# Optimization experiments

Hardware: AMD Instinct MI355X
Metric: run time of the kernel (lower is better)

Reference implementation:

```python
import jax, jax.numpy as jnp
import numpy as np

N = 100000      # num nodes
E = 800000      # num edges
IN = 128        # in_channels
OUT = 128       # out_channels
ALPHA = 0.5


def setup_inputs() -> dict:
    key = jax.random.key(0)
    k1, k2, k3, k4, k5, k6 = jax.random.split(key, 6)
    x = jax.random.normal(k1, (N, IN), dtype=jnp.float32)
    edge_index = jax.random.randint(k2, (2, E), 0, N, dtype=jnp.int32)
    # GCNConv linear weights (glorot-ish) and biases for both directions
    s = 1.0 / np.sqrt(IN)
    W_sd = jax.random.normal(k3, (IN, OUT), dtype=jnp.float32) * s
    b_sd = jnp.zeros((OUT,), dtype=jnp.float32)
    W_ds = jax.random.normal(k4, (IN, OUT), dtype=jnp.float32) * s
    b_ds = jnp.zeros((OUT,), dtype=jnp.float32)
    return {"x": x, "edge_index": edge_index, "W_sd": W_sd, "b_sd": b_sd,
            "W_ds": W_ds, "b_ds": b_ds}


def _dir_gcn_norm_weights(row, col, dtype):
    """edge_weight = out_deg_inv_sqrt[row] * in_deg_inv_sqrt[col] (unit input weights)."""
    ones = jnp.ones((row.shape[0],), dtype=dtype)
    in_deg = jax.ops.segment_sum(ones, col, num_segments=N)
    out_deg = jax.ops.segment_sum(ones, row, num_segments=N)
    in_inv = jnp.where(in_deg > 0, jax.lax.rsqrt(in_deg), 0.0).astype(dtype)
    out_inv = jnp.where(out_deg > 0, jax.lax.rsqrt(out_deg), 0.0).astype(dtype)
    return out_inv[row] * in_inv[col]


def _gcn_conv(x, W, b, src, dst, w):
    """GCNConv(normalize=False, add_self_loops=False): lin -> gather -> scale -> scatter-add -> +bias."""
    h = x @ W                                   # [N, OUT]
    msg = h[src] * w[:, None]                   # [E, OUT]
    return jax.ops.segment_sum(msg, dst, num_segments=N) + b


def reference(x, edge_index, W_sd, b_sd, W_ds, b_ds):
    row, col = edge_index[0], edge_index[1]
    # forward-direction norm (src->dst) and transposed-graph norm (edge_index.flip(0))
    w = _dir_gcn_norm_weights(row, col, x.dtype)
    w_t = _dir_gcn_norm_weights(col, row, x.dtype)
    # conv_dst_to_src uses transposed edges: source=col, dest=row
    x_in = _gcn_conv(x, W_ds, b_ds, col, row, w_t)
    # conv_src_to_dst uses original edges: source=row, dest=col
    x_out = _gcn_conv(x, W_sd, b_sd, row, col, w)
    return ALPHA * x_in + (1.0 - ALPHA) * x_out
```

## Files before the change

### kernel.cpp

```cpp
#include <hip/hip_runtime.h>

#define NN 100000
#define NE 800000
#define NI 1600000
#define NB 391
#define IPB 6250

#define GB_CVT 12500
#define GB_PW  128
#define GB_HIST 256

#define OFF_INV    0u
#define OFF_OFFS   800000u
#define OFF_BB     1600008u
#define OFF_HIST   1601600u
#define OFF_CSRC   2001984u
#define OFF_XB     8401984u
#define OFF_PAIRS  34001984u
#define OFF_WT     85201984u
#define OFF_BIAS   85267520u
#define OFF_TOT    85268032u

typedef short short8 __attribute__((ext_vector_type(8)));
typedef unsigned short u16x8 __attribute__((ext_vector_type(8)));
typedef float f32x4 __attribute__((ext_vector_type(4)));
typedef float f32x8 __attribute__((ext_vector_type(8)));

__device__ __forceinline__ unsigned short f2bf(float f) {
    unsigned u = __float_as_uint(f);
    u = (u + 0x7FFFu + ((u >> 16) & 1u)) >> 16;
    return (unsigned short)u;
}
__device__ __forceinline__ float b2f(unsigned short h) {
    return __uint_as_float(((unsigned)h) << 16);
}
__device__ __forceinline__ f32x8 bvec2f(u16x8 v) {
    f32x8 r;
#pragma unroll
    for (int i = 0; i < 8; ++i) r[i] = b2f(v[i]);
    return r;
}


__global__ __launch_bounds__(256) void k_prep(
    const float4* __restrict__ x4, ushort4* __restrict__ xb4,
    const float* __restrict__ Wds, const float* __restrict__ Wsd,
    const float* __restrict__ bds, const float* __restrict__ bsd,
    unsigned short* __restrict__ wt, float* __restrict__ bias,
    const int* __restrict__ ei, int* __restrict__ hist) {
    __shared__ int h[NB];
    int bid = blockIdx.x;
    if (bid < GB_CVT) {
        int i = bid * 256 + threadIdx.x;
        float4 v = x4[i];
        ushort4 o;
        o.x = f2bf(v.x); o.y = f2bf(v.y); o.z = f2bf(v.z); o.w = f2bf(v.w);
        xb4[i] = o;
        return;
    }
    if (bid < GB_CVT + GB_PW) {
        int id = (bid - GB_CVT) * 256 + threadIdx.x;
        int c = id & 127;
        int k = id >> 7;
        float v = (k < 128) ? Wds[k * 128 + c] : Wsd[(k - 128) * 128 + c];
        wt[c * 256 + k] = f2bf(v);
        if (k == 0) bias[c] = 0.5f * (bds[c] + bsd[c]);
        return;
    }
    int hb = bid - GB_CVT - GB_PW;
    for (int k = threadIdx.x; k < NB; k += 256) h[k] = 0;
    __syncthreads();
    int base = hb * IPB;
    for (int t = threadIdx.x; t < IPB; t += 256) {
        int i = base + t;
        int key = (i < NE) ? ei[i] : (NN + ei[i]);
        atomicAdd(&h[key >> 9], 1);
    }
    __syncthreads();
    for (int k = threadIdx.x; k < NB; k += 256) hist[k * 256 + hb] = h[k];
}

__global__ __launch_bounds__(256) void k_red(const int* __restrict__ hist,
                                             int* __restrict__ tot) {
    __shared__ int s[256];
    int k = blockIdx.x;
    s[threadIdx.x] = hist[k * 256 + threadIdx.x];
    __syncthreads();
    for (int st = 128; st > 0; st >>= 1) {
        if (threadIdx.x < st) s[threadIdx.x] += s[threadIdx.x + st];
        __syncthreads();
    }
    if (threadIdx.x == 0) tot[k] = s[0];
}

__global__ __launch_bounds__(512) void k_scan_tot(const int* __restrict__ tot,
                                                  int* __restrict__ bb) {
    __shared__ int sA[512], sB[512];
    int tid = threadIdx.x;
    int v = (tid < NB) ? tot[tid] : 0;
    sA[tid] = v;
    __syncthreads();
    int *src = sA, *dst = sB;
    for (int st = 1; st < 512; st <<= 1) {
        dst[tid] = src[tid] + ((tid >= st) ? src[tid - st] : 0);
        __syncthreads();
        int* tp = src; src = dst; dst = tp;
    }
    if (tid <= NB) bb[tid] = (tid > 0) ? src[tid - 1] : 0;
}

__global__ __launch_bounds__(256) void k_rebase(int* __restrict__ hist,
                                                const int* __restrict__ bb) {
    __shared__ int sA[256], sB[256];
    int k = blockIdx.x, tid = threadIdx.x;
    int v = hist[k * 256 + tid];
    sA[tid] = v;
    __syncthreads();
    int *src = sA, *dst = sB;
    for (int st = 1; st < 256; st <<= 1) {
        dst[tid] = src[tid] + ((tid >= st) ? src[tid - st] : 0);
        __syncthreads();
        int* tp = src; src = dst; dst = tp;
    }
    hist[k * 256 + tid] = bb[k] + src[tid] - v;
}

__global__ __launch_bounds__(256) void k_scatter(const int* __restrict__ ei,
                                                 const int* __restrict__ hist,
                                                 unsigned long long* __restrict__ pairs) {
    __shared__ int cur[NB];
    for (int k = threadIdx.x; k < NB; k += 256) cur[k] = hist[k * 256 + blockIdx.x];
    __syncthreads();
    int base = blockIdx.x * IPB;
    for (int t = threadIdx.x; t < IPB; t += 256) {
        int i = base + t;
        int e = ei[i];
        int key, val;
        if (i < NE) { key = e;      val = ei[NE + i]; }
        else        { key = NN + e; val = ei[i - NE]; }
        int pos = atomicAdd(&cur[key >> 9], 1);
        pairs[pos] = (((unsigned long long)(unsigned)key) << 32) | (unsigned)val;
    }
}

__global__ __launch_bounds__(256) void k_bucket(const unsigned long long* __restrict__ pairs,
                                                const int* __restrict__ bb,
                                                int* __restrict__ csr_src,
                                                int* __restrict__ offsets,
                                                float* __restrict__ inv) {
    __shared__ int sA[512], sB[512], cur[512];
    const int h = blockIdx.x, tid = threadIdx.x;
    const int s0 = bb[h], s1 = bb[h + 1];
    for (int k = tid; k < 512; k += 256) sA[k] = 0;
    __syncthreads();
    for (int i = s0 + tid; i < s1; i += 256) {
        int key = (int)(pairs[i] >> 32);
        atomicAdd(&sA[key & 511], 1);
    }
    __syncthreads();
    int *src = sA, *dst = sB;
    for (int st = 1; st < 512; st <<= 1) {
        for (int k = tid; k < 512; k += 256) dst[k] = src[k] + ((k >= st) ? src[k - st] : 0);
        __syncthreads();
        int* tp = src; src = dst; dst = tp;
    }
    for (int k = tid; k < 512; k += 256) {
        int incl = src[k];
        int excl = (k > 0) ? src[k - 1] : 0;
        cur[k] = s0 + excl;
        int gkey = h * 512 + k;
        if (gkey <= 2 * NN) offsets[gkey] = s0 + excl;
        if (gkey < 2 * NN) {
            int cnt = incl - excl;
            inv[gkey] = (cnt > 0) ? rsqrtf((float)cnt) : 0.0f;
        }
    }
    __syncthreads();
    for (int i = s0 + tid; i < s1; i += 256) {
        unsigned long long p = pairs[i];
        int key = (int)(p >> 32);
        int pos = atomicAdd(&cur[key & 511], 1);
        csr_src[pos] = (int)(unsigned)(p & 0xffffffffULL);
    }
}

__global__ __launch_bounds__(512) void k_gather_gemm(
    const u16x8* __restrict__ xb8, const int* __restrict__ offsets,
    const int* __restrict__ csr_src, const float* __restrict__ inv,
    const unsigned short* __restrict__ wt, const float* __restrict__ bias,
    float* __restrict__ out) {
    __shared__ unsigned short a_lds[32][264];

    const int g = threadIdx.x >> 4;
    const int cl = threadIdx.x & 15;
    const int n0 = blockIdx.x * 32;

#pragma unroll
    for (int i = 0; i < 2; ++i) {
        const int seg = g + 32 * i;
        const int nl = seg >> 1;
        const int dir = seg & 1;
        const int n = n0 + nl;

        const int key = dir * NN + n;
        int s0 = offsets[key], s1 = offsets[key + 1];
        const float* __restrict__ srcinv = inv + (dir ^ 1) * NN;

        f32x8 acc = {0.f, 0.f, 0.f, 0.f, 0.f, 0.f, 0.f, 0.f};
        int e = s0;
        for (; e + 4 <= s1; e += 4) {
            int i0 = csr_src[e];
            int i1 = csr_src[e + 1];
            int i2 = csr_src[e + 2];
            int i3 = csr_src[e + 3];
            float w0 = srcinv[i0], w1 = srcinv[i1], w2 = srcinv[i2], w3 = srcinv[i3];
            u16x8 v0 = xb8[i0 * 16 + cl];
            u16x8 v1 = xb8[i1 * 16 + cl];
            u16x8 v2 = xb8[i2 * 16 + cl];
            u16x8 v3 = xb8[i3 * 16 + cl];
            acc += w0 * bvec2f(v0);
            acc += w1 * bvec2f(v1);
            acc += w2 * bvec2f(v2);
            acc += w3 * bvec2f(v3);
        }
        for (; e < s1; ++e) {
            int i0 = csr_src[e];
            float w0 = srcinv[i0];
            u16x8 v0 = xb8[i0 * 16 + cl];
            acc += w0 * bvec2f(v0);
        }

        float ds = 0.5f * inv[dir * NN + n];
        u16x8 o;
#pragma unroll
        for (int j = 0; j < 8; ++j) o[j] = f2bf(acc[j] * ds);
        *(u16x8*)&a_lds[nl][dir * 128 + cl * 8] = o;
    }
    __syncthreads();

    const int wave = threadIdx.x >> 6;
    const int lane = threadIdx.x & 63;
    const int fr = lane & 15;
    const int kg = (lane >> 4) * 8;
    const int rt = wave & 1;
    const int ct0 = (wave >> 1) * 2;

    f32x4 acc[2] = {};
#pragma unroll
    for (int s = 0; s < 8; ++s) {
        short8 afrag = *(const short8*)&a_lds[rt * 16 + fr][s * 32 + kg];
#pragma unroll
        for (int c = 0; c < 2; ++c) {
            short8 bfrag = *(const short8*)(wt + ((ct0 + c) * 16 + fr) * 256 + s * 32 + kg);
            acc[c] = __builtin_amdgcn_mfma_f32_16x16x32_bf16(afrag, bfrag, acc[c], 0, 0, 0);
        }
    }

    const int orow0 = n0 + rt * 16 + (lane >> 4) * 4;
#pragma unroll
    for (int c = 0; c < 2; ++c) {
        const int col = (ct0 + c) * 16 + fr;
        const float b = bias[col];
#pragma unroll
        for (int i = 0; i < 4; ++i) {
            out[(orow0 + i) * 128 + col] = acc[c][i] + b;
        }
    }
}

extern "C" void kernel_launch(void* const* d_in, const int* in_sizes, int n_in,
                              void* d_out, int out_size, void* d_ws, size_t ws_size,
                              hipStream_t stream) {
    const float* x   = (const float*)d_in[0];
    const int* ei    = (const int*)d_in[1];
    const float* Wsd = (const float*)d_in[2];
    const float* bsd = (const float*)d_in[3];
    const float* Wds = (const float*)d_in[4];
    const float* bds = (const float*)d_in[5];

    char* ws = (char*)d_ws;
    float* inv     = (float*)(ws + OFF_INV);
    int*   offsets = (int*)(ws + OFF_OFFS);
    int*   bb      = (int*)(ws + OFF_BB);
    int*   hist    = (int*)(ws + OFF_HIST);
    int*   csr_src = (int*)(ws + OFF_CSRC);
    unsigned short* xb  = (unsigned short*)(ws + OFF_XB);
    unsigned long long* pairs = (unsigned long long*)(ws + OFF_PAIRS);
    unsigned short* wt  = (unsigned short*)(ws + OFF_WT);
    float* bias    = (float*)(ws + OFF_BIAS);
    int*   tot     = (int*)(ws + OFF_TOT);

    k_prep<<<GB_CVT + GB_PW + GB_HIST, 256, 0, stream>>>(
        (const float4*)x, (ushort4*)xb, Wds, Wsd, bds, bsd, wt, bias, ei, hist);
    k_red<<<NB, 256, 0, stream>>>(hist, tot);
    k_scan_tot<<<1, 512, 0, stream>>>(tot, bb);
    k_rebase<<<NB, 256, 0, stream>>>(hist, bb);
    k_scatter<<<256, 256, 0, stream>>>(ei, hist, pairs);
    k_bucket<<<NB, 256, 0, stream>>>(pairs, bb, csr_src, offsets, inv);
    k_gather_gemm<<<NN / 32, 512, 0, stream>>>((const u16x8*)xb, offsets, csr_src, inv,
                                               wt, bias, (float*)d_out);
}
```

Before: 189.3 us.

## Interleave two gather segments per thread group and halve gather-gemm block size

```diff
diff --git a/kernel.cpp b/kernel.cpp
--- a/kernel.cpp
+++ b/kernel.cpp
@@ -184,57 +184,100 @@
     }
 }
 
-__global__ __launch_bounds__(512) void k_gather_gemm(
+__global__ __launch_bounds__(256) void k_gather_gemm(
     const u16x8* __restrict__ xb8, const int* __restrict__ offsets,
     const int* __restrict__ csr_src, const float* __restrict__ inv,
     const unsigned short* __restrict__ wt, const float* __restrict__ bias,
     float* __restrict__ out) {
-    __shared__ unsigned short a_lds[32][264];
+    __shared__ unsigned short a_lds[16][264];
 
     const int g = threadIdx.x >> 4;
     const int cl = threadIdx.x & 15;
-    const int n0 = blockIdx.x * 32;
-
-#pragma unroll
-    for (int i = 0; i < 2; ++i) {
-        const int seg = g + 32 * i;
-        const int nl = seg >> 1;
-        const int dir = seg & 1;
-        const int n = n0 + nl;
-
-        const int key = dir * NN + n;
-        int s0 = offsets[key], s1 = offsets[key + 1];
-        const float* __restrict__ srcinv = inv + (dir ^ 1) * NN;
-
-        f32x8 acc = {0.f, 0.f, 0.f, 0.f, 0.f, 0.f, 0.f, 0.f};
-        int e = s0;
-        for (; e + 4 <= s1; e += 4) {
-            int i0 = csr_src[e];
-            int i1 = csr_src[e + 1];
-            int i2 = csr_src[e + 2];
-            int i3 = csr_src[e + 3];
-            float w0 = srcinv[i0], w1 = srcinv[i1], w2 = srcinv[i2], w3 = srcinv[i3];
-            u16x8 v0 = xb8[i0 * 16 + cl];
-            u16x8 v1 = xb8[i1 * 16 + cl];
-            u16x8 v2 = xb8[i2 * 16 + cl];
-            u16x8 v3 = xb8[i3 * 16 + cl];
-            acc += w0 * bvec2f(v0);
-            acc += w1 * bvec2f(v1);
-            acc += w2 * bvec2f(v2);
-            acc += w3 * bvec2f(v3);
-        }
-        for (; e < s1; ++e) {
-            int i0 = csr_src[e];
-            float w0 = srcinv[i0];
-            u16x8 v0 = xb8[i0 * 16 + cl];
-            acc += w0 * bvec2f(v0);
-        }
-
-        float ds = 0.5f * inv[dir * NN + n];
-        u16x8 o;
-#pragma unroll
-        for (int j = 0; j < 8; ++j) o[j] = f2bf(acc[j] * ds);
-        *(u16x8*)&a_lds[nl][dir * 128 + cl * 8] = o;
+    const int n0 = blockIdx.x * 16;
+
+    const int nlA = g >> 1,        dirA = g & 1;
+    const int nlB = (g + 16) >> 1, dirB = g & 1;
+    const int nA = n0 + nlA, nB = n0 + nlB;
+
+    int eA = offsets[dirA * NN + nA], endA = offsets[dirA * NN + nA + 1];
+    int eB = offsets[dirB * NN + nB], endB = offsets[dirB * NN + nB + 1];
+    const float* __restrict__ invA = inv + (dirA ^ 1) * NN;
+    const float* __restrict__ invB = inv + (dirB ^ 1) * NN;
+
+    f32x8 accA = {0.f, 0.f, 0.f, 0.f, 0.f, 0.f, 0.f, 0.f};
+    f32x8 accB = {0.f, 0.f, 0.f, 0.f, 0.f, 0.f, 0.f, 0.f};
+
+    while (eA + 4 <= endA && eB + 4 <= endB) {
+        int a0 = csr_src[eA], a1 = csr_src[eA + 1], a2 = csr_src[eA + 2], a3 = csr_src[eA + 3];
+        int b0 = csr_src[eB], b1 = csr_src[eB + 1], b2 = csr_src[eB + 2], b3 = csr_src[eB + 3];
+        float wa0 = invA[a0], wa1 = invA[a1], wa2 = invA[a2], wa3 = invA[a3];
+        float wb0 = invB[b0], wb1 = invB[b1], wb2 = invB[b2], wb3 = invB[b3];
+        u16x8 va0 = xb8[a0 * 16 + cl];
+        u16x8 va1 = xb8[a1 * 16 + cl];
+        u16x8 va2 = xb8[a2 * 16 + cl];
+        u16x8 va3 = xb8[a3 * 16 + cl];
+        u16x8 vb0 = xb8[b0 * 16 + cl];
+        u16x8 vb1 = xb8[b1 * 16 + cl];
+        u16x8 vb2 = xb8[b2 * 16 + cl];
+        u16x8 vb3 = xb8[b3 * 16 + cl];
+        accA += wa0 * bvec2f(va0);
+        accA += wa1 * bvec2f(va1);
+        accA += wa2 * bvec2f(va2);
+        accA += wa3 * bvec2f(va3);
+        accB += wb0 * bvec2f(vb0);
+        accB += wb1 * bvec2f(vb1);
+        accB += wb2 * bvec2f(vb2);
+        accB += wb3 * bvec2f(vb3);
+        eA += 4; eB += 4;
+    }
+    for (; eA + 4 <= endA; eA += 4) {
+        int a0 = csr_src[eA], a1 = csr_src[eA + 1], a2 = csr_src[eA + 2], a3 = csr_src[eA + 3];
+        float w0 = invA[a0], w1 = invA[a1], w2 = invA[a2], w3 = invA[a3];
+        u16x8 v0 = xb8[a0 * 16 + cl];
+        u16x8 v1 = xb8[a1 * 16 + cl];
+        u16x8 v2 = xb8[a2 * 16 + cl];
+        u16x8 v3 = xb8[a3 * 16 + cl];
+        accA += w0 * bvec2f(v0);
+        accA += w1 * bvec2f(v1);
+        accA += w2 * bvec2f(v2);
+        accA += w3 * bvec2f(v3);
+    }
+    for (; eA < endA; ++eA) {
+        int a0 = csr_src[eA];
+        float w0 = invA[a0];
+        u16x8 v0 = xb8[a0 * 16 + cl];
+        accA += w0 * bvec2f(v0);
+    }
+    for (; eB + 4 <= endB; eB += 4) {
+        int b0 = csr_src[eB], b1 = csr_src[eB + 1], b2 = csr_src[eB + 2], b3 = csr_src[eB + 3];
+        float w0 = invB[b0], w1 = invB[b1], w2 = invB[b2], w3 = invB[b3];
+        u16x8 v0 = xb8[b0 * 16 + cl];
+        u16x8 v1 = xb8[b1 * 16 + cl];
+        u16x8 v2 = xb8[b2 * 16 + cl];
+        u16x8 v3 = xb8[b3 * 16 + cl];
+        accB += w0 * bvec2f(v0);
+        accB += w1 * bvec2f(v1);
+        accB += w2 * bvec2f(v2);
+        accB += w3 * bvec2f(v3);
+    }
+    for (; eB < endB; ++eB) {
+        int b0 = csr_src[eB];
+        float w0 = invB[b0];
+        u16x8 v0 = xb8[b0 * 16 + cl];
+        accB += w0 * bvec2f(v0);
+    }
+
+    {
+        float dsA = 0.5f * inv[dirA * NN + nA];
+        u16x8 oA;
+#pragma unroll
+        for (int j = 0; j < 8; ++j) oA[j] = f2bf(accA[j] * dsA);
+        *(u16x8*)&a_lds[nlA][dirA * 128 + cl * 8] = oA;
+        float dsB = 0.5f * inv[dirB * NN + nB];
+        u16x8 oB;
+#pragma unroll
+        for (int j = 0; j < 8; ++j) oB[j] = f2bf(accB[j] * dsB);
+        *(u16x8*)&a_lds[nlB][dirB * 128 + cl * 8] = oB;
     }
     __syncthreads();
 
@@ -242,13 +285,12 @@
     const int lane = threadIdx.x & 63;
     const int fr = lane & 15;
     const int kg = (lane >> 4) * 8;
-    const int rt = wave & 1;
-    const int ct0 = (wave >> 1) * 2;
+    const int ct0 = wave * 2;
 
     f32x4 acc[2] = {};
 #pragma unroll
     for (int s = 0; s < 8; ++s) {
-        short8 afrag = *(const short8*)&a_lds[rt * 16 + fr][s * 32 + kg];
+        short8 afrag = *(const short8*)&a_lds[fr][s * 32 + kg];
 #pragma unroll
         for (int c = 0; c < 2; ++c) {
             short8 bfrag = *(const short8*)(wt + ((ct0 + c) * 16 + fr) * 256 + s * 32 + kg);
@@ -256,7 +298,7 @@
         }
     }
 
-    const int orow0 = n0 + rt * 16 + (lane >> 4) * 4;
+    const int orow0 = n0 + (lane >> 4) * 4;
 #pragma unroll
     for (int c = 0; c < 2; ++c) {
         const int col = (ct0 + c) * 16 + fr;
@@ -297,6 +339,6 @@
     k_rebase<<<NB, 256, 0, stream>>>(hist, bb);
     k_scatter<<<256, 256, 0, stream>>>(ei, hist, pairs);
     k_bucket<<<NB, 256, 0, stream>>>(pairs, bb, csr_src, offsets, inv);
-    k_gather_gemm<<<NN / 32, 512, 0, stream>>>((const u16x8*)xb, offsets, csr_src, inv,
+    k_gather_gemm<<<NN / 16, 256, 0, stream>>>((const u16x8*)xb, offsets, csr_src, inv,
                                                wt, bias, (float*)d_out);
 }
```

Result: slower. 200.0 us (+5.7%).

## Sort nodes by degree for gather-GEMM, pack pairs to 32-bit, merge scan kernels

Applied to the files above, without the earlier changes.

```diff
diff --git a/kernel.cpp b/kernel.cpp
--- a/kernel.cpp
+++ b/kernel.cpp
@@ -9,6 +9,8 @@
 #define GB_CVT 12500
 #define GB_PW  128
 #define GB_HIST 256
+
+#define DB 196
 
 #define OFF_INV    0u
 #define OFF_OFFS   800000u
@@ -20,6 +22,9 @@
 #define OFF_WT     85201984u
 #define OFF_BIAS   85267520u
 #define OFF_TOT    85268032u
+#define OFF_ORD    85269600u
+#define OFF_DH     85669600u
+#define OFF_DT     85931744u
 
 typedef short short8 __attribute__((ext_vector_type(8)));
 typedef unsigned short u16x8 __attribute__((ext_vector_type(8)));
@@ -80,17 +85,21 @@
     for (int k = threadIdx.x; k < NB; k += 256) hist[k * 256 + hb] = h[k];
 }
 
-__global__ __launch_bounds__(256) void k_red(const int* __restrict__ hist,
-                                             int* __restrict__ tot) {
-    __shared__ int s[256];
-    int k = blockIdx.x;
-    s[threadIdx.x] = hist[k * 256 + threadIdx.x];
-    __syncthreads();
-    for (int st = 128; st > 0; st >>= 1) {
-        if (threadIdx.x < st) s[threadIdx.x] += s[threadIdx.x + st];
-        __syncthreads();
-    }
-    if (threadIdx.x == 0) tot[k] = s[0];
+__global__ __launch_bounds__(256) void k_colscan(int* __restrict__ hist,
+                                                 int* __restrict__ tot) {
+    __shared__ int sA[256], sB[256];
+    int k = blockIdx.x, tid = threadIdx.x;
+    int v = hist[k * 256 + tid];
+    sA[tid] = v;
+    __syncthreads();
+    int *src = sA, *dst = sB;
+    for (int st = 1; st < 256; st <<= 1) {
+        dst[tid] = src[tid] + ((tid >= st) ? src[tid - st] : 0);
+        __syncthreads();
+        int* tp = src; src = dst; dst = tp;
+    }
+    hist[k * 256 + tid] = src[tid] - v;
+    if (tid == 255) tot[k] = src[255];
 }
 
 __global__ __launch_bounds__(512) void k_scan_tot(const int* __restrict__ tot,
@@ -109,27 +118,13 @@
     if (tid <= NB) bb[tid] = (tid > 0) ? src[tid - 1] : 0;
 }
 
-__global__ __launch_bounds__(256) void k_rebase(int* __restrict__ hist,
-                                                const int* __restrict__ bb) {
-    __shared__ int sA[256], sB[256];
-    int k = blockIdx.x, tid = threadIdx.x;
-    int v = hist[k * 256 + tid];
-    sA[tid] = v;
-    __syncthreads();
-    int *src = sA, *dst = sB;
-    for (int st = 1; st < 256; st <<= 1) {
-        dst[tid] = src[tid] + ((tid >= st) ? src[tid - st] : 0);
-        __syncthreads();
-        int* tp = src; src = dst; dst = tp;
-    }
-    hist[k * 256 + tid] = bb[k] + src[tid] - v;
-}
-
 __global__ __launch_bounds__(256) void k_scatter(const int* __restrict__ ei,
                                                  const int* __restrict__ hist,
-                                                 unsigned long long* __restrict__ pairs) {
+                                                 const int* __restrict__ bb,
+                                                 unsigned int* __restrict__ pairs) {
     __shared__ int cur[NB];
-    for (int k = threadIdx.x; k < NB; k += 256) cur[k] = hist[k * 256 + blockIdx.x];
+    for (int k = threadIdx.x; k < NB; k += 256)
+        cur[k] = bb[k] + hist[k * 256 + blockIdx.x];
     __syncthreads();
     int base = blockIdx.x * IPB;
     for (int t = threadIdx.x; t < IPB; t += 256) {
@@ -139,11 +134,11 @@
         if (i < NE) { key = e;      val = ei[NE + i]; }
         else        { key = NN + e; val = ei[i - NE]; }
         int pos = atomicAdd(&cur[key >> 9], 1);
-        pairs[pos] = (((unsigned long long)(unsigned)key) << 32) | (unsigned)val;
-    }
-}
-
-__global__ __launch_bounds__(256) void k_bucket(const unsigned long long* __restrict__ pairs,
+        pairs[pos] = ((unsigned)val << 9) | (unsigned)(key & 511);
+    }
+}
+
+__global__ __launch_bounds__(256) void k_bucket(const unsigned int* __restrict__ pairs,
                                                 const int* __restrict__ bb,
                                                 int* __restrict__ csr_src,
                                                 int* __restrict__ offsets,
@@ -154,8 +149,7 @@
     for (int k = tid; k < 512; k += 256) sA[k] = 0;
     __syncthreads();
     for (int i = s0 + tid; i < s1; i += 256) {
-        int key = (int)(pairs[i] >> 32);
-        atomicAdd(&sA[key & 511], 1);
+        atomicAdd(&sA[pairs[i] & 511], 1);
     }
     __syncthreads();
     int *src = sA, *dst = sB;
@@ -177,10 +171,68 @@
     }
     __syncthreads();
     for (int i = s0 + tid; i < s1; i += 256) {
-        unsigned long long p = pairs[i];
-        int key = (int)(p >> 32);
-        int pos = atomicAdd(&cur[key & 511], 1);
-        csr_src[pos] = (int)(unsigned)(p & 0xffffffffULL);
+        unsigned int p = pairs[i];
+        int pos = atomicAdd(&cur[p & 511], 1);
+        csr_src[pos] = (int)(p >> 9);
+    }
+}
+
+__global__ __launch_bounds__(512) void k_dh(const int* __restrict__ offsets,
+                                            int* __restrict__ dhist) {
+    __shared__ int lh[256];
+    int b = blockIdx.x, t = threadIdx.x;
+    if (t < 256) lh[t] = 0;
+    __syncthreads();
+    int n = b * 512 + t;
+    if (n < NN) {
+        int d = (offsets[n + 1] - offsets[n]) + (offsets[NN + n + 1] - offsets[NN + n]);
+        int bin = d > 255 ? 255 : d;
+        atomicAdd(&lh[bin], 1);
+    }
+    __syncthreads();
+    if (t < 256) dhist[t * 256 + b] = lh[t];
+}
+
+__global__ __launch_bounds__(256) void k_dcol(int* __restrict__ dhist,
+                                              int* __restrict__ dtot) {
+    __shared__ int sA[256], sB[256];
+    int k = blockIdx.x, tid = threadIdx.x;
+    int v = (tid < DB) ? dhist[k * 256 + tid] : 0;
+    sA[tid] = v;
+    __syncthreads();
+    int *src = sA, *dst = sB;
+    for (int st = 1; st < 256; st <<= 1) {
+        dst[tid] = src[tid] + ((tid >= st) ? src[tid - st] : 0);
+        __syncthreads();
+        int* tp = src; src = dst; dst = tp;
+    }
+    dhist[k * 256 + tid] = src[tid] - v;
+    if (tid == 255) dtot[k] = src[255];
+}
+
+__global__ __launch_bounds__(512) void k_dorder(const int* __restrict__ offsets,
+                                                const int* __restrict__ dhist,
+                                                const int* __restrict__ dtot,
+                                                int* __restrict__ order) {
+    __shared__ int sc[256], cur[256];
+    int b = blockIdx.x, t = threadIdx.x;
+    if (t < 256) sc[t] = dtot[t];
+    __syncthreads();
+    for (int st = 1; st < 256; st <<= 1) {
+        int v = 0;
+        if (t < 256 && t >= st) v = sc[t - st];
+        __syncthreads();
+        if (t < 256) sc[t] += v;
+        __syncthreads();
+    }
+    if (t < 256) cur[t] = (sc[t] - dtot[t]) + dhist[t * 256 + b];
+    __syncthreads();
+    int n = b * 512 + t;
+    if (n < NN) {
+        int d = (offsets[n + 1] - offsets[n]) + (offsets[NN + n + 1] - offsets[NN + n]);
+        int bin = d > 255 ? 255 : d;
+        int pos = atomicAdd(&cur[bin], 1);
+        order[pos] = n;
     }
 }
 
@@ -188,26 +240,21 @@
     const u16x8* __restrict__ xb8, const int* __restrict__ offsets,
     const int* __restrict__ csr_src, const float* __restrict__ inv,
     const unsigned short* __restrict__ wt, const float* __restrict__ bias,
-    float* __restrict__ out) {
+    const int* __restrict__ order, float* __restrict__ out) {
     __shared__ unsigned short a_lds[32][264];
+    __shared__ int nid[32];
 
     const int g = threadIdx.x >> 4;
     const int cl = threadIdx.x & 15;
-    const int n0 = blockIdx.x * 32;
-
-#pragma unroll
-    for (int i = 0; i < 2; ++i) {
-        const int seg = g + 32 * i;
-        const int nl = seg >> 1;
-        const int dir = seg & 1;
-        const int n = n0 + nl;
-
-        const int key = dir * NN + n;
-        int s0 = offsets[key], s1 = offsets[key + 1];
+    const int nd = order[blockIdx.x * 32 + g];
+    if (cl == 0) nid[g] = nd;
+
+#pragma unroll
+    for (int dir = 0; dir < 2; ++dir) {
+        int e = offsets[dir * NN + nd], s1 = offsets[dir * NN + nd + 1];
         const float* __restrict__ srcinv = inv + (dir ^ 1) * NN;
 
         f32x8 acc = {0.f, 0.f, 0.f, 0.f, 0.f, 0.f, 0.f, 0.f};
-        int e = s0;
         for (; e + 4 <= s1; e += 4) {
             int i0 = csr_src[e];
             int i1 = csr_src[e + 1];
@@ -230,11 +277,11 @@
             acc += w0 * bvec2f(v0);
         }
 
-        float ds = 0.5f * inv[dir * NN + n];
+        float ds = 0.5f * inv[dir * NN + nd];
         u16x8 o;
 #pragma unroll
         for (int j = 0; j < 8; ++j) o[j] = f2bf(acc[j] * ds);
-        *(u16x8*)&a_lds[nl][dir * 128 + cl * 8] = o;
+        *(u16x8*)&a_lds[g][dir * 128 + cl * 8] = o;
     }
     __syncthreads();
 
@@ -256,14 +303,14 @@
         }
     }
 
-    const int orow0 = n0 + rt * 16 + (lane >> 4) * 4;
+    const int orow_l = rt * 16 + (lane >> 4) * 4;
 #pragma unroll
     for (int c = 0; c < 2; ++c) {
         const int col = (ct0 + c) * 16 + fr;
         const float b = bias[col];
 #pragma unroll
         for (int i = 0; i < 4; ++i) {
-            out[(orow0 + i) * 128 + col] = acc[c][i] + b;
+            out[nid[orow_l + i] * 128 + col] = acc[c][i] + b;
         }
     }
 }
@@ -285,18 +332,23 @@
     int*   hist    = (int*)(ws + OFF_HIST);
     int*   csr_src = (int*)(ws + OFF_CSRC);
     unsigned short* xb  = (unsigned short*)(ws + OFF_XB);
-    unsigned long long* pairs = (unsigned long long*)(ws + OFF_PAIRS);
+    unsigned int* pairs = (unsigned int*)(ws + OFF_PAIRS);
     unsigned short* wt  = (unsigned short*)(ws + OFF_WT);
     float* bias    = (float*)(ws + OFF_BIAS);
     int*   tot     = (int*)(ws + OFF_TOT);
+    int*   order   = (int*)(ws + OFF_ORD);
+    int*   dhist   = (int*)(ws + OFF_DH);
+    int*   dtot    = (int*)(ws + OFF_DT);
 
     k_prep<<<GB_CVT + GB_PW + GB_HIST, 256, 0, stream>>>(
         (const float4*)x, (ushort4*)xb, Wds, Wsd, bds, bsd, wt, bias, ei, hist);
-    k_red<<<NB, 256, 0, stream>>>(hist, tot);
+    k_colscan<<<NB, 256, 0, stream>>>(hist, tot);
     k_scan_tot<<<1, 512, 0, stream>>>(tot, bb);
-    k_rebase<<<NB, 256, 0, stream>>>(hist, bb);
-    k_scatter<<<256, 256, 0, stream>>>(ei, hist, pairs);
+    k_scatter<<<256, 256, 0, stream>>>(ei, hist, bb, pairs);
     k_bucket<<<NB, 256, 0, stream>>>(pairs, bb, csr_src, offsets, inv);
+    k_dh<<<DB, 512, 0, stream>>>(offsets, dhist);
+    k_dcol<<<256, 256, 0, stream>>>(dhist, dtot);
+    k_dorder<<<DB, 512, 0, stream>>>(offsets, dhist, dtot, order);
     k_gather_gemm<<<NN / 32, 512, 0, stream>>>((const u16x8*)xb, offsets, csr_src, inv,
-                                               wt, bias, (float*)d_out);
-}
+                                               wt, bias, order, (float*)d_out);
+}
```

Measured after the change: 198.9 us. +5.1%, slower.
